# Optimization experiments

Hardware: AMD Instinct MI355X
Metric: run time of the kernel (lower is better)

## Reference

```python
import jax, jax.numpy as jnp
import numpy as np

BATCH, NUM_TREE, TOTAL_NODES, WIDTH = 256, 64, 341, 4  # depth=4 -> 1024 leaves


def setup_inputs() -> dict:
    key = jax.random.key(0)
    inputs = jax.random.normal(key, (BATCH, NUM_TREE, TOTAL_NODES, WIDTH), dtype=jnp.float32)
    return {"inputs": inputs}


def reference(inputs):
    """Soft decision forest: per-node softmax over `width` branches, leaf prob =
    product of branch probs along the root->leaf path. Node indices follow the
    original DFS preorder; leaves are emitted in DFS order.
    Input: [B, T, total_nodes, width] -> Output: [B, T, width**(depth+1)].
    """
    B, T, N, W = inputs.shape
    # invert total_nodes = sum_{z=0}^{depth} W^z  (same formula as _depth_calc)
    depth = int(round(np.log(1 - N * (1 - W)) / np.log(W) - 1))
    D = depth + 1  # number of internal levels traversed (call uses depth+1)

    P = jax.nn.softmax(inputs, axis=-1)  # [B, T, N, W]

    w = jnp.ones((B, T, 1), dtype=inputs.dtype)  # leaf-prefix weights
    idx = np.zeros(1, dtype=np.int64)            # DFS node indices for current level
    for l in range(D):
        probs = jnp.take(P, jnp.asarray(idx), axis=2)      # [B, T, K, W]
        w = (w[..., None] * probs).reshape(B, T, -1)        # [B, T, K*W]
        # child j of preorder node i with (D-l-1) remaining levels below child:
        # child_idx = i + 1 + j * s(D-l-1), s(m) = (W^m - 1)/(W - 1)
        s_child = (W ** (D - 1 - l) - 1) // (W - 1)
        idx = (idx[:, None] + 1 + np.arange(W, dtype=np.int64) * s_child).reshape(-1)
    return w  # [B, T, W**D]
```

## Files before the change

### kernel.cpp

```cpp
#include <hip/hip_runtime.h>


#define NUM_NODES 341

__global__ __launch_bounds__(256) void forest_kernel(const float* __restrict__ in,
                                                     float* __restrict__ out) {
    __shared__ float4 sP[NUM_NODES];

    const int bt  = blockIdx.x;
    const int tid = threadIdx.x;

    const float4* in4 = reinterpret_cast<const float4*>(in) + (size_t)bt * NUM_NODES;
    for (int n = tid; n < NUM_NODES; n += 256) {
        float4 v = in4[n];
        float m  = fmaxf(fmaxf(v.x, v.y), fmaxf(v.z, v.w));
        float e0 = __expf(v.x - m);
        float e1 = __expf(v.y - m);
        float e2 = __expf(v.z - m);
        float e3 = __expf(v.w - m);
        float r  = 1.0f / (e0 + e1 + e2 + e3);
        sP[n] = make_float4(e0 * r, e1 * r, e2 * r, e3 * r);
    }
    __syncthreads();

    const float* sPf = reinterpret_cast<const float*>(sP);
    const int j0 =  tid >> 6;
    const int j1 = (tid >> 4) & 3;
    const int j2 = (tid >> 2) & 3;
    const int j3 =  tid & 3;

    const int n1 = 1 + j0 * 85;
    const int n2 = n1 + 1 + j1 * 21;
    const int n3 = n2 + 1 + j2 * 5;
    const int n4 = n3 + 1 + j3;

    const float pre = sPf[j0]
                    * sPf[n1 * 4 + j1]
                    * sPf[n2 * 4 + j2]
                    * sPf[n3 * 4 + j3];

    float4 pv = sP[n4];
    float4 o  = make_float4(pre * pv.x, pre * pv.y, pre * pv.z, pre * pv.w);

    reinterpret_cast<float4*>(out)[(size_t)bt * 256 + tid] = o;
}

extern "C" void kernel_launch(void* const* d_in, const int* in_sizes, int n_in,
                              void* d_out, int out_size, void* d_ws, size_t ws_size,
                              hipStream_t stream) {
    const float* in = (const float*)d_in[0];
    float* out = (float*)d_out;
    const int num_bt = 256 * 64;
    forest_kernel<<<num_bt, 256, 0, stream>>>(in, out);
}
```

Baseline: 28.37 us.

## Assign one (batch,tree) per wavefront and drop block-wide barrier

Each 256-thread block now handles four (batch,tree) pairs, one per wavefront, with a private shared-memory slice per wave. The block-level __syncthreads is replaced by an LDS wait plus a scheduling barrier, which relies on a wave's LDS writes being visible to its own lanes in program order. Each lane issues all six of its input loads up front for more memory-level parallelism, then writes four output float4s. The aim is to remove block-wide synchronisation stalls and the idle threads left by the 341-node strided loop, at the cost of more registers and four times the shared memory per block.

```diff
diff --git a/kernel.cpp b/kernel.cpp
--- a/kernel.cpp
+++ b/kernel.cpp
@@ -5,44 +5,62 @@
 
 __global__ __launch_bounds__(256) void forest_kernel(const float* __restrict__ in,
                                                      float* __restrict__ out) {
-    __shared__ float4 sP[NUM_NODES];
+    __shared__ float4 sP[4][NUM_NODES];
 
-    const int bt  = blockIdx.x;
-    const int tid = threadIdx.x;
+    const int tid  = threadIdx.x;
+    const int wave = tid >> 6;
+    const int lane = tid & 63;
+    const int bt   = blockIdx.x * 4 + wave;
+
+    float4* sPw = sP[wave];
+    const float* sPf = reinterpret_cast<const float*>(sPw);
 
     const float4* in4 = reinterpret_cast<const float4*>(in) + (size_t)bt * NUM_NODES;
-    for (int n = tid; n < NUM_NODES; n += 256) {
-        float4 v = in4[n];
-        float m  = fmaxf(fmaxf(v.x, v.y), fmaxf(v.z, v.w));
-        float e0 = __expf(v.x - m);
-        float e1 = __expf(v.y - m);
-        float e2 = __expf(v.z - m);
-        float e3 = __expf(v.w - m);
-        float r  = 1.0f / (e0 + e1 + e2 + e3);
-        sP[n] = make_float4(e0 * r, e1 * r, e2 * r, e3 * r);
+    float4 v[6];
+#pragma unroll
+    for (int i = 0; i < 5; ++i) v[i] = in4[lane + 64 * i];
+    const bool tail = (lane < NUM_NODES - 320);
+    if (tail) v[5] = in4[lane + 320];
+
+#pragma unroll
+    for (int i = 0; i < 6; ++i) {
+        if (i < 5 || tail) {
+            float4 x = v[i];
+            float m  = fmaxf(fmaxf(x.x, x.y), fmaxf(x.z, x.w));
+            float e0 = __expf(x.x - m);
+            float e1 = __expf(x.y - m);
+            float e2 = __expf(x.z - m);
+            float e3 = __expf(x.w - m);
+            float r  = 1.0f / (e0 + e1 + e2 + e3);
+            sPw[lane + 64 * i] = make_float4(e0 * r, e1 * r, e2 * r, e3 * r);
+        }
     }
-    __syncthreads();
 
-    const float* sPf = reinterpret_cast<const float*>(sP);
-    const int j0 =  tid >> 6;
-    const int j1 = (tid >> 4) & 3;
-    const int j2 = (tid >> 2) & 3;
-    const int j3 =  tid & 3;
+    asm volatile("s_waitcnt lgkmcnt(0)" ::: "memory");
+    __builtin_amdgcn_sched_barrier(0);
 
-    const int n1 = 1 + j0 * 85;
-    const int n2 = n1 + 1 + j1 * 21;
-    const int n3 = n2 + 1 + j2 * 5;
-    const int n4 = n3 + 1 + j3;
+    const int j1 = lane >> 4;
+    const int j2 = (lane >> 2) & 3;
+    const int j3 = lane & 3;
 
-    const float pre = sPf[j0]
-                    * sPf[n1 * 4 + j1]
-                    * sPf[n2 * 4 + j2]
-                    * sPf[n3 * 4 + j3];
+    float4* out4 = reinterpret_cast<float4*>(out) + (size_t)bt * 256;
 
-    float4 pv = sP[n4];
-    float4 o  = make_float4(pre * pv.x, pre * pv.y, pre * pv.z, pre * pv.w);
+#pragma unroll
+    for (int j0 = 0; j0 < 4; ++j0) {
+        const int n1 = 1 + 85 * j0;
+        const int n2 = n1 + 1 + 21 * j1;
+        const int n3 = n2 + 1 + 5 * j2;
+        const int n4 = n3 + 1 + j3;
 
-    reinterpret_cast<float4*>(out)[(size_t)bt * 256 + tid] = o;
+        const float pre = sPf[j0]
+                        * sPf[n1 * 4 + j1]
+                        * sPf[n2 * 4 + j2]
+                        * sPf[n3 * 4 + j3];
+
+        float4 pv = sPw[n4];
+        out4[j0 * 64 + lane] = make_float4(pre * pv.x, pre * pv.y,
+                                           pre * pv.z, pre * pv.w);
+    }
 }
 
 extern "C" void kernel_launch(void* const* d_in, const int* in_sizes, int n_in,
@@ -50,6 +68,6 @@
                               hipStream_t stream) {
     const float* in = (const float*)d_in[0];
     float* out = (float*)d_out;
-    const int num_bt = 256 * 64;
-    forest_kernel<<<num_bt, 256, 0, stream>>>(in, out);
+    const int num_blocks = (256 * 64) / 4;
+    forest_kernel<<<num_blocks, 256, 0, stream>>>(in, out);
 }
```

New measurement: 28.62 us. About the same (+0.9%).

## Make forest kernel persistent with register prefetch and double-buffered shared memory

Applied to the files above, without the earlier changes.

Launches a fixed grid of 2048 blocks that each process 8 batch-tree items in a loop. The next item's input is prefetched into registers while the current one is computed, and a double-buffered shared array lets each iteration use a single barrier. The aim is to overlap global loads with compute and cut block launch overhead. In exchange, fewer blocks are resident, which may lower memory-level parallelism on a bandwidth-bound kernel.

```diff
diff --git a/kernel.cpp b/kernel.cpp
--- a/kernel.cpp
+++ b/kernel.cpp
@@ -2,47 +2,70 @@
 
 
 #define NUM_NODES 341
+#define GRID 2048
+#define ITERS 8
 
 __global__ __launch_bounds__(256) void forest_kernel(const float* __restrict__ in,
                                                      float* __restrict__ out) {
-    __shared__ float4 sP[NUM_NODES];
+    __shared__ float4 sP[2][NUM_NODES];
 
-    const int bt  = blockIdx.x;
     const int tid = threadIdx.x;
+    const bool tail = (tid < NUM_NODES - 256);
 
-    const float4* in4 = reinterpret_cast<const float4*>(in) + (size_t)bt * NUM_NODES;
-    for (int n = tid; n < NUM_NODES; n += 256) {
-        float4 v = in4[n];
-        float m  = fmaxf(fmaxf(v.x, v.y), fmaxf(v.z, v.w));
-        float e0 = __expf(v.x - m);
-        float e1 = __expf(v.y - m);
-        float e2 = __expf(v.z - m);
-        float e3 = __expf(v.w - m);
-        float r  = 1.0f / (e0 + e1 + e2 + e3);
-        sP[n] = make_float4(e0 * r, e1 * r, e2 * r, e3 * r);
-    }
-    __syncthreads();
-
-    const float* sPf = reinterpret_cast<const float*>(sP);
     const int j0 =  tid >> 6;
     const int j1 = (tid >> 4) & 3;
     const int j2 = (tid >> 2) & 3;
     const int j3 =  tid & 3;
-
     const int n1 = 1 + j0 * 85;
     const int n2 = n1 + 1 + j1 * 21;
     const int n3 = n2 + 1 + j2 * 5;
     const int n4 = n3 + 1 + j3;
 
-    const float pre = sPf[j0]
-                    * sPf[n1 * 4 + j1]
-                    * sPf[n2 * 4 + j2]
-                    * sPf[n3 * 4 + j3];
+    const float4* in4 = reinterpret_cast<const float4*>(in);
+    size_t bt = blockIdx.x;
+    float4 v0 = in4[bt * NUM_NODES + tid];
+    float4 v1 = tail ? in4[bt * NUM_NODES + 256 + tid] : make_float4(0, 0, 0, 0);
 
-    float4 pv = sP[n4];
-    float4 o  = make_float4(pre * pv.x, pre * pv.y, pre * pv.z, pre * pv.w);
+    int buf = 0;
+#pragma unroll
+    for (int i = 0; i < ITERS; ++i) {
+        {
+            float4 x = v0;
+            float m  = fmaxf(fmaxf(x.x, x.y), fmaxf(x.z, x.w));
+            float e0 = __expf(x.x - m), e1 = __expf(x.y - m);
+            float e2 = __expf(x.z - m), e3 = __expf(x.w - m);
+            float r  = 1.0f / (e0 + e1 + e2 + e3);
+            sP[buf][tid] = make_float4(e0 * r, e1 * r, e2 * r, e3 * r);
+        }
+        if (tail) {
+            float4 x = v1;
+            float m  = fmaxf(fmaxf(x.x, x.y), fmaxf(x.z, x.w));
+            float e0 = __expf(x.x - m), e1 = __expf(x.y - m);
+            float e2 = __expf(x.z - m), e3 = __expf(x.w - m);
+            float r  = 1.0f / (e0 + e1 + e2 + e3);
+            sP[buf][256 + tid] = make_float4(e0 * r, e1 * r, e2 * r, e3 * r);
+        }
 
-    reinterpret_cast<float4*>(out)[(size_t)bt * 256 + tid] = o;
+        if (i < ITERS - 1) {
+            const size_t btn = bt + GRID;
+            v0 = in4[btn * NUM_NODES + tid];
+            if (tail) v1 = in4[btn * NUM_NODES + 256 + tid];
+        }
+
+        __syncthreads();
+
+        const float* sPf = reinterpret_cast<const float*>(sP[buf]);
+        const float pre = sPf[j0]
+                        * sPf[n1 * 4 + j1]
+                        * sPf[n2 * 4 + j2]
+                        * sPf[n3 * 4 + j3];
+        float4 pv = sP[buf][n4];
+        reinterpret_cast<float4*>(out)[bt * 256 + tid] =
+            make_float4(pre * pv.x, pre * pv.y, pre * pv.z, pre * pv.w);
+
+        bt += GRID;
+        buf ^= 1;
+    }
 }
 
 extern "C" void kernel_launch(void* const* d_in, const int* in_sizes, int n_in,
@@ -50,6 +73,5 @@
                               hipStream_t stream) {
     const float* in = (const float*)d_in[0];
     float* out = (float*)d_out;
-    const int num_bt = 256 * 64;
-    forest_kernel<<<num_bt, 256, 0, stream>>>(in, out);
+    forest_kernel<<<GRID, 256, 0, stream>>>(in, out);
 }
```

After: 29.46 us. +3.8%, slower.
